# Optimization experiments

Measured on AMD Instinct MI355X. Metric: run time of the kernel, lower is better.

## Reference

```python
import jax, jax.numpy as jnp
import numpy as np

N, PAIR, M, D, O, R = 4096, 2, 64, 128, 128, 2
MAX_DEG = 32


def setup_inputs() -> dict:
    key = jax.random.key(0)
    k1, k2, k3, k4, k5, k6 = jax.random.split(key, 6)
    node_features = jax.random.normal(k1, (N, PAIR, M, D), dtype=jnp.float32)
    deg = jax.random.randint(k2, (N,), 0, MAX_DEG, dtype=jnp.int32)
    # per-relation Linear params (stored as [in, out]) and self-loop Linear
    W_r = jax.random.normal(k3, (R, D, O), dtype=jnp.float32) / np.sqrt(D)
    b_r = jax.random.normal(k4, (R, O), dtype=jnp.float32) * 0.01
    W0 = jax.random.normal(k5, (D, O), dtype=jnp.float32) / np.sqrt(D)
    b0 = jax.random.normal(k6, (O,), dtype=jnp.float32) * 0.01
    return {"node_features": node_features, "deg": deg, "W_r": W_r,
            "b_r": b_r, "W0": W0, "b0": b0}


def reference(node_features, deg, W_r, b_r, W0, b0):
    # Original: for each relation r, for each neighbor, adds W_r(x_i);
    # i.e. sum_r deg_i * (x_i @ W_r + b_r) = deg_i * (x_i @ sum_r W_r + sum_r b_r)
    Wsum = W_r.sum(axis=0)          # [D, O]
    bsum = b_r.sum(axis=0)          # [O]
    rel = jnp.einsum('npmd,do->npmo', node_features, Wsum) + bsum
    self_term = jnp.einsum('npmd,do->npmo', node_features, W0) + b0
    d = deg.astype(node_features.dtype)[:, None, None, None]
    h = jax.nn.relu(d * rel + self_term)  # [N, 2, M, O]
    # edge representation: mm(h_i, h_j.T) per entity -> [N, M, M]
    out = jnp.einsum('nmo,nko->nmk', h[:, 0], h[:, 1])
    return out
```

## Files before the change

kernel.cpp:

```cpp
#include <hip/hip_runtime.h>
#include <hip/hip_bf16.h>


typedef __attribute__((ext_vector_type(8))) short bf16x8;
typedef __attribute__((ext_vector_type(4))) float f32x4;

__device__ __forceinline__ unsigned int pkbf(float a, float b) {
    union { __hip_bfloat162 h; unsigned int u; } v;
    v.h = __float22bfloat162_rn(float2{a, b});
    return v.u;
}

__global__ __launch_bounds__(256) void build_weights(
    const float* __restrict__ W_r,
    const float* __restrict__ b_r,
    const float* __restrict__ W0,
    const float* __restrict__ b0,
    unsigned short* __restrict__ wfrag,
    float* __restrict__ call)
{
    int t = blockIdx.x * blockDim.x + threadIdx.x;
    int lane = t & 63;
    int ks = (t >> 6) & 3;
    int ct = (t >> 8) & 7;
    int d  = (t >> 11) & 31;
    int o = ct * 16 + (lane & 15);
    int kbase = ks * 32 + (lane >> 4) * 8;
    unsigned int* dst = (unsigned int*)(wfrag + (size_t)t * 8);
#pragma unroll
    for (int j = 0; j < 4; ++j) {
        int k0 = kbase + 2 * j;
        float wA = (float)d * (W_r[k0 * 128 + o] + W_r[128 * 128 + k0 * 128 + o]) + W0[k0 * 128 + o];
        float wB = (float)d * (W_r[(k0 + 1) * 128 + o] + W_r[128 * 128 + (k0 + 1) * 128 + o]) + W0[(k0 + 1) * 128 + o];
        dst[j] = pkbf(wA, wB);
    }
    if (t < 32 * 128) {
        int dd = t >> 7, oo = t & 127;
        call[t] = (float)dd * (b_r[oo] + b_r[128 + oo]) + b0[oo];
    }
}

__global__ __launch_bounds__(256, 4) void edge_kernel(
    const float* __restrict__ x,
    const int* __restrict__ deg,
    const unsigned short* __restrict__ wfrag,
    const float* __restrict__ call,
    float* __restrict__ out)
{
    __shared__ char ldsb[33280];

    const int n = blockIdx.x;
    const int tid = threadIdx.x;
    const int wave = tid >> 6;
    const int lane = tid & 63;
    const int l15 = lane & 15;
    const int lhi = lane >> 4;
    const int d = deg[n];

    const float* xn = x + (size_t)n * (2 * 64 * 128);
    const char* wsrc = (const char*)(wfrag + (size_t)d * (8 * 4 * 64 * 8));
    const float* cd = call + d * 128;

#pragma unroll
    for (int i = 0; i < 8; ++i) {
        __builtin_amdgcn_global_load_lds(
            (const __attribute__((address_space(1))) unsigned int*)(wsrc + (size_t)i * 4096 + (size_t)tid * 16),
            (__attribute__((address_space(3))) unsigned int*)(ldsb + i * 4096 + wave * 1024),
            16, 0, 0);
    }
    if (tid < 32) {
        __builtin_amdgcn_global_load_lds(
            (const __attribute__((address_space(1))) unsigned int*)(cd + tid * 4),
            (__attribute__((address_space(3))) unsigned int*)(ldsb + 32768),
            16, 0, 0);
    }

    const int rbase = wave * 32;
    const float* r0p = xn + (size_t)(rbase + l15) * 128 + lhi * 8;
    const float* r1p = r0p + (size_t)16 * 128;
    bf16x8 afrag[2][4];
    f32x4 ring[4][2];
#pragma unroll
    for (int u = 0; u < 4; ++u) {
        const f32x4* p = (const f32x4*)(r0p + (u & 3) * 32);
        ring[u][0] = p[0];
        ring[u][1] = p[1];
    }
#pragma unroll
    for (int u = 0; u < 8; ++u) {
        f32x4 a0 = ring[u & 3][0];
        f32x4 a1 = ring[u & 3][1];
        if (u < 4) {
            const f32x4* p = (const f32x4*)(r1p + (u & 3) * 32);
            ring[u & 3][0] = p[0];
            ring[u & 3][1] = p[1];
        }
        union { bf16x8 vv; unsigned int uu[4]; } f;
        f.uu[0] = pkbf(a0.x, a0.y);
        f.uu[1] = pkbf(a0.z, a0.w);
        f.uu[2] = pkbf(a1.x, a1.y);
        f.uu[3] = pkbf(a1.z, a1.w);
        afrag[u >> 2][u & 3] = f.vv;
        __builtin_amdgcn_sched_barrier(0);
    }

    __syncthreads();

#pragma unroll
    for (int ct = 0; ct < 8; ++ct) {
        bf16x8 bfrag[4];
#pragma unroll
        for (int ks = 0; ks < 4; ++ks)
            bfrag[ks] = *(const bf16x8*)(ldsb + ct * 4096 + ks * 1024 + lane * 16);
        f32x4 acc[2] = {{0.f,0.f,0.f,0.f},{0.f,0.f,0.f,0.f}};
#pragma unroll
        for (int ks = 0; ks < 4; ++ks)
#pragma unroll
            for (int rt = 0; rt < 2; ++rt)
                acc[rt] = __builtin_amdgcn_mfma_f32_16x16x32_bf16(bfrag[ks], afrag[rt][ks], acc[rt], 0, 0, 0);
        const f32x4 cc4 = *(const f32x4*)(ldsb + 32768 + ct * 64 + lhi * 16);

        __syncthreads();

#pragma unroll
        for (int rt = 0; rt < 2; ++rt) {
            const int m = rbase + rt * 16 + l15;
            const int slot = ((lhi >> 1) ^ ((m >> 2) & 1));
            float h0v = fmaxf(acc[rt][0] + cc4.x, 0.f);
            float h1v = fmaxf(acc[rt][1] + cc4.y, 0.f);
            float h2v = fmaxf(acc[rt][2] + cc4.z, 0.f);
            float h3v = fmaxf(acc[rt][3] + cc4.w, 0.f);
            union { unsigned int u[2]; unsigned long long ull; } pk;
            pk.u[0] = pkbf(h0v, h1v);
            pk.u[1] = pkbf(h2v, h3v);
            *(unsigned long long*)(ldsb + ct * 4096 + m * 32 + slot * 16 + (lhi & 1) * 8) = pk.ull;
        }
    }
    __syncthreads();

    const int mrow = wave * 16 + l15;
    bf16x8 hb[4];
#pragma unroll
    for (int ks = 0; ks < 4; ++ks) {
        const int ct = ks * 2 + (lhi >> 1);
        const int s  = (lhi & 1) ^ ((mrow >> 2) & 1);
        hb[ks] = *(const bf16x8*)(ldsb + ct * 4096 + mrow * 32 + s * 16);
    }
    float* outn = out + (size_t)n * 4096;
#pragma unroll
    for (int qt = 0; qt < 4; ++qt) {
        const int qrow = 64 + qt * 16 + l15;
        f32x4 acc = {0.f, 0.f, 0.f, 0.f};
#pragma unroll
        for (int ks = 0; ks < 4; ++ks) {
            const int ct = ks * 2 + (lhi >> 1);
            const int s  = (lhi & 1) ^ ((qrow >> 2) & 1);
            bf16x8 ha = *(const bf16x8*)(ldsb + ct * 4096 + qrow * 32 + s * 16);
            acc = __builtin_amdgcn_mfma_f32_16x16x32_bf16(ha, hb[ks], acc, 0, 0, 0);
        }
        *(f32x4*)(outn + mrow * 64 + qt * 16 + lhi * 4) = acc;
    }
}

extern "C" void kernel_launch(void* const* d_in, const int* in_sizes, int n_in,
                              void* d_out, int out_size, void* d_ws, size_t ws_size,
                              hipStream_t stream) {
    const float* x   = (const float*)d_in[0];
    const int*   deg = (const int*)d_in[1];
    const float* W_r = (const float*)d_in[2];
    const float* b_r = (const float*)d_in[3];
    const float* W0  = (const float*)d_in[4];
    const float* b0  = (const float*)d_in[5];
    float* out = (float*)d_out;

    unsigned short* wfrag = (unsigned short*)d_ws;
    float* call = (float*)((unsigned short*)d_ws + 32 * 8 * 4 * 64 * 8);

    build_weights<<<256, 256, 0, stream>>>(W_r, b_r, W0, b0, wfrag, call);
    edge_kernel<<<4096, 256, 0, stream>>>(x, deg, wfrag, call, out);
}
```

Measured before the change: 74.99 us.

## Process four nodes per block with prefetched x loads and raw barriers

Each block now handles four consecutive nodes in a loop. The next node's x rows are issued into registers while the current node's second MFMA stage runs, so global latency overlaps compute. Some __syncthreads are replaced by raw s_barrier with an lgkmcnt wait, which avoids waiting on outstanding vmem loads. The grid shrinks to a quarter of its size, which lowers parallelism and raises register pressure from the extra xraw buffer.

```diff
diff --git a/kernel.cpp b/kernel.cpp
--- a/kernel.cpp
+++ b/kernel.cpp
@@ -4,6 +4,12 @@
 
 typedef __attribute__((ext_vector_type(8))) short bf16x8;
 typedef __attribute__((ext_vector_type(4))) float f32x4;
+
+#define RAW_BARRIER() do {                                   \
+    asm volatile("s_waitcnt lgkmcnt(0)" ::: "memory");       \
+    __builtin_amdgcn_s_barrier();                            \
+    __builtin_amdgcn_sched_barrier(0);                       \
+} while (0)
 
 __device__ __forceinline__ unsigned int pkbf(float a, float b) {
     union { __hip_bfloat162 h; unsigned int u; } v;
@@ -49,116 +55,134 @@
 {
     __shared__ char ldsb[33280];
 
-    const int n = blockIdx.x;
     const int tid = threadIdx.x;
     const int wave = tid >> 6;
     const int lane = tid & 63;
     const int l15 = lane & 15;
     const int lhi = lane >> 4;
-    const int d = deg[n];
-
-    const float* xn = x + (size_t)n * (2 * 64 * 128);
-    const char* wsrc = (const char*)(wfrag + (size_t)d * (8 * 4 * 64 * 8));
-    const float* cd = call + d * 128;
-
-#pragma unroll
-    for (int i = 0; i < 8; ++i) {
-        __builtin_amdgcn_global_load_lds(
-            (const __attribute__((address_space(1))) unsigned int*)(wsrc + (size_t)i * 4096 + (size_t)tid * 16),
-            (__attribute__((address_space(3))) unsigned int*)(ldsb + i * 4096 + wave * 1024),
-            16, 0, 0);
-    }
-    if (tid < 32) {
-        __builtin_amdgcn_global_load_lds(
-            (const __attribute__((address_space(1))) unsigned int*)(cd + tid * 4),
-            (__attribute__((address_space(3))) unsigned int*)(ldsb + 32768),
-            16, 0, 0);
-    }
-
     const int rbase = wave * 32;
-    const float* r0p = xn + (size_t)(rbase + l15) * 128 + lhi * 8;
-    const float* r1p = r0p + (size_t)16 * 128;
+    const int nb = blockIdx.x * 4;
+
+    int dg[4];
+#pragma unroll
+    for (int j = 0; j < 4; ++j) dg[j] = deg[nb + j];
+
+    f32x4 xraw[2][4][2];
     bf16x8 afrag[2][4];
-    f32x4 ring[4][2];
-#pragma unroll
-    for (int u = 0; u < 4; ++u) {
-        const f32x4* p = (const f32x4*)(r0p + (u & 3) * 32);
-        ring[u][0] = p[0];
-        ring[u][1] = p[1];
-    }
-#pragma unroll
-    for (int u = 0; u < 8; ++u) {
-        f32x4 a0 = ring[u & 3][0];
-        f32x4 a1 = ring[u & 3][1];
-        if (u < 4) {
-            const f32x4* p = (const f32x4*)(r1p + (u & 3) * 32);
-            ring[u & 3][0] = p[0];
-            ring[u & 3][1] = p[1];
-        }
-        union { bf16x8 vv; unsigned int uu[4]; } f;
-        f.uu[0] = pkbf(a0.x, a0.y);
-        f.uu[1] = pkbf(a0.z, a0.w);
-        f.uu[2] = pkbf(a1.x, a1.y);
-        f.uu[3] = pkbf(a1.z, a1.w);
-        afrag[u >> 2][u & 3] = f.vv;
-        __builtin_amdgcn_sched_barrier(0);
-    }
-
+
+    auto stage_w = [&](int d) {
+        const char* wsrc = (const char*)(wfrag + (size_t)d * (8 * 4 * 64 * 8));
+#pragma unroll
+        for (int i = 0; i < 8; ++i) {
+            __builtin_amdgcn_global_load_lds(
+                (const __attribute__((address_space(1))) unsigned int*)(wsrc + (size_t)i * 4096 + (size_t)tid * 16),
+                (__attribute__((address_space(3))) unsigned int*)(ldsb + i * 4096 + wave * 1024),
+                16, 0, 0);
+        }
+        if (tid < 32) {
+            __builtin_amdgcn_global_load_lds(
+                (const __attribute__((address_space(1))) unsigned int*)(call + d * 128 + tid * 4),
+                (__attribute__((address_space(3))) unsigned int*)(ldsb + 32768),
+                16, 0, 0);
+        }
+    };
+    auto issue_x = [&](int n) {
+        const float* r0p = x + (size_t)n * 16384 + (size_t)(rbase + l15) * 128 + lhi * 8;
+#pragma unroll
+        for (int rt = 0; rt < 2; ++rt)
+#pragma unroll
+            for (int ks = 0; ks < 4; ++ks) {
+                const f32x4* p = (const f32x4*)(r0p + rt * 2048 + ks * 32);
+                xraw[rt][ks][0] = p[0];
+                xraw[rt][ks][1] = p[1];
+            }
+    };
+    auto convert_x = [&]() {
+#pragma unroll
+        for (int rt = 0; rt < 2; ++rt)
+#pragma unroll
+            for (int ks = 0; ks < 4; ++ks) {
+                f32x4 a0 = xraw[rt][ks][0];
+                f32x4 a1 = xraw[rt][ks][1];
+                union { bf16x8 v; unsigned int u[4]; } f;
+                f.u[0] = pkbf(a0.x, a0.y);
+                f.u[1] = pkbf(a0.z, a0.w);
+                f.u[2] = pkbf(a1.x, a1.y);
+                f.u[3] = pkbf(a1.z, a1.w);
+                afrag[rt][ks] = f.v;
+            }
+    };
+
+    stage_w(dg[0]);
+    issue_x(nb);
+    convert_x();
     __syncthreads();
 
-#pragma unroll
-    for (int ct = 0; ct < 8; ++ct) {
-        bf16x8 bfrag[4];
-#pragma unroll
-        for (int ks = 0; ks < 4; ++ks)
-            bfrag[ks] = *(const bf16x8*)(ldsb + ct * 4096 + ks * 1024 + lane * 16);
-        f32x4 acc[2] = {{0.f,0.f,0.f,0.f},{0.f,0.f,0.f,0.f}};
-#pragma unroll
-        for (int ks = 0; ks < 4; ++ks)
-#pragma unroll
-            for (int rt = 0; rt < 2; ++rt)
-                acc[rt] = __builtin_amdgcn_mfma_f32_16x16x32_bf16(bfrag[ks], afrag[rt][ks], acc[rt], 0, 0, 0);
-        const f32x4 cc4 = *(const f32x4*)(ldsb + 32768 + ct * 64 + lhi * 16);
-
-        __syncthreads();
-
-#pragma unroll
-        for (int rt = 0; rt < 2; ++rt) {
-            const int m = rbase + rt * 16 + l15;
-            const int slot = ((lhi >> 1) ^ ((m >> 2) & 1));
-            float h0v = fmaxf(acc[rt][0] + cc4.x, 0.f);
-            float h1v = fmaxf(acc[rt][1] + cc4.y, 0.f);
-            float h2v = fmaxf(acc[rt][2] + cc4.z, 0.f);
-            float h3v = fmaxf(acc[rt][3] + cc4.w, 0.f);
-            union { unsigned int u[2]; unsigned long long ull; } pk;
-            pk.u[0] = pkbf(h0v, h1v);
-            pk.u[1] = pkbf(h2v, h3v);
-            *(unsigned long long*)(ldsb + ct * 4096 + m * 32 + slot * 16 + (lhi & 1) * 8) = pk.ull;
-        }
-    }
-    __syncthreads();
-
-    const int mrow = wave * 16 + l15;
-    bf16x8 hb[4];
-#pragma unroll
-    for (int ks = 0; ks < 4; ++ks) {
-        const int ct = ks * 2 + (lhi >> 1);
-        const int s  = (lhi & 1) ^ ((mrow >> 2) & 1);
-        hb[ks] = *(const bf16x8*)(ldsb + ct * 4096 + mrow * 32 + s * 16);
-    }
-    float* outn = out + (size_t)n * 4096;
-#pragma unroll
-    for (int qt = 0; qt < 4; ++qt) {
-        const int qrow = 64 + qt * 16 + l15;
-        f32x4 acc = {0.f, 0.f, 0.f, 0.f};
+    for (int j = 0; j < 4; ++j) {
+#pragma unroll
+        for (int ct = 0; ct < 8; ++ct) {
+            bf16x8 bfrag[4];
+#pragma unroll
+            for (int ks = 0; ks < 4; ++ks)
+                bfrag[ks] = *(const bf16x8*)(ldsb + ct * 4096 + ks * 1024 + lane * 16);
+            f32x4 acc[2] = {{0.f,0.f,0.f,0.f},{0.f,0.f,0.f,0.f}};
+#pragma unroll
+            for (int ks = 0; ks < 4; ++ks)
+#pragma unroll
+                for (int rt = 0; rt < 2; ++rt)
+                    acc[rt] = __builtin_amdgcn_mfma_f32_16x16x32_bf16(bfrag[ks], afrag[rt][ks], acc[rt], 0, 0, 0);
+            const f32x4 cc4 = *(const f32x4*)(ldsb + 32768 + ct * 64 + lhi * 16);
+
+            RAW_BARRIER();
+
+#pragma unroll
+            for (int rt = 0; rt < 2; ++rt) {
+                const int m = rbase + rt * 16 + l15;
+                const int slot = ((lhi >> 1) ^ ((m >> 2) & 1));
+                float h0v = fmaxf(acc[rt][0] + cc4.x, 0.f);
+                float h1v = fmaxf(acc[rt][1] + cc4.y, 0.f);
+                float h2v = fmaxf(acc[rt][2] + cc4.z, 0.f);
+                float h3v = fmaxf(acc[rt][3] + cc4.w, 0.f);
+                union { unsigned int u[2]; unsigned long long ull; } pk;
+                pk.u[0] = pkbf(h0v, h1v);
+                pk.u[1] = pkbf(h2v, h3v);
+                *(unsigned long long*)(ldsb + ct * 4096 + m * 32 + slot * 16 + (lhi & 1) * 8) = pk.ull;
+            }
+        }
+        RAW_BARRIER();
+
+        if (j < 3) issue_x(nb + j + 1);
+
+        const int mrow = wave * 16 + l15;
+        bf16x8 hb[4];
 #pragma unroll
         for (int ks = 0; ks < 4; ++ks) {
             const int ct = ks * 2 + (lhi >> 1);
-            const int s  = (lhi & 1) ^ ((qrow >> 2) & 1);
-            bf16x8 ha = *(const bf16x8*)(ldsb + ct * 4096 + qrow * 32 + s * 16);
-            acc = __builtin_amdgcn_mfma_f32_16x16x32_bf16(ha, hb[ks], acc, 0, 0, 0);
-        }
-        *(f32x4*)(outn + mrow * 64 + qt * 16 + lhi * 4) = acc;
+            const int s  = (lhi & 1) ^ ((mrow >> 2) & 1);
+            hb[ks] = *(const bf16x8*)(ldsb + ct * 4096 + mrow * 32 + s * 16);
+        }
+        float* outn = out + (size_t)(nb + j) * 4096;
+#pragma unroll
+        for (int qt = 0; qt < 4; ++qt) {
+            const int qrow = 64 + qt * 16 + l15;
+            f32x4 acc = {0.f, 0.f, 0.f, 0.f};
+#pragma unroll
+            for (int ks = 0; ks < 4; ++ks) {
+                const int ct = ks * 2 + (lhi >> 1);
+                const int s  = (lhi & 1) ^ ((qrow >> 2) & 1);
+                bf16x8 ha = *(const bf16x8*)(ldsb + ct * 4096 + qrow * 32 + s * 16);
+                acc = __builtin_amdgcn_mfma_f32_16x16x32_bf16(ha, hb[ks], acc, 0, 0, 0);
+            }
+            *(f32x4*)(outn + mrow * 64 + qt * 16 + lhi * 4) = acc;
+        }
+
+        RAW_BARRIER();
+
+        if (j < 3) {
+            stage_w(dg[j + 1]);
+            convert_x();
+            __syncthreads();
+        }
     }
 }
 
@@ -177,5 +201,5 @@
     float* call = (float*)((unsigned short*)d_ws + 32 * 8 * 4 * 64 * 8);
 
     build_weights<<<256, 256, 0, stream>>>(W_r, b_r, W0, b0, wfrag, call);
-    edge_kernel<<<4096, 256, 0, stream>>>(x, deg, wfrag, call, out);
-}
+    edge_kernel<<<1024, 256, 0, stream>>>(x, deg, wfrag, call, out);
+}
```

New measurement: 82.13 us. +9.5%, slower.
